# Kernel optimization log

Hardware: AMD Instinct MI355X
Metric: run time of the kernel (lower is better)

Reference implementation:

```python
import jax, jax.numpy as jnp
import numpy as np

N = 100000      # nodes
E = 1600000     # edges (before self loops)
F_IN = 128      # input features
HID = 64        # hidden_layer (heads=1)
G = 128         # number of graphs
NUM_CLASSES = 10


def _gat_layer(x, src, dst, W, a_src, a_dst, b):
    # x: [N, Fin] -> h: [N, HID]; single head, PyG GATConv defaults
    h = x @ W
    alpha_src = h @ a_src            # [N]
    alpha_dst = h @ a_dst            # [N]
    e = jax.nn.leaky_relu(alpha_src[src] + alpha_dst[dst], 0.2)   # [E+N]
    # segment softmax over incoming edges of each destination node
    m = jax.ops.segment_max(e, dst, num_segments=N)
    ex = jnp.exp(e - m[dst])
    denom = jax.ops.segment_sum(ex, dst, num_segments=N)
    alpha = ex / denom[dst]
    out = jax.ops.segment_sum(h[src] * alpha[:, None], dst, num_segments=N)
    return out + b


def setup_inputs() -> dict:
    key = jax.random.key(0)
    ks = jax.random.split(key, 16)
    x = jax.random.normal(ks[0], (N, F_IN), dtype=jnp.float32)
    edge_index = jax.random.randint(ks[1], (2, E), 0, N, dtype=jnp.int64)
    edge_weight = jax.random.uniform(ks[2], (E,), dtype=jnp.float32)
    batch = jnp.sort(jax.random.randint(ks[3], (N,), 0, G, dtype=jnp.int64))
    s = 0.1
    params = {
        'W1': jax.random.normal(ks[4], (F_IN, HID), jnp.float32) * s,
        'a_src1': jax.random.normal(ks[5], (HID,), jnp.float32) * s,
        'a_dst1': jax.random.normal(ks[6], (HID,), jnp.float32) * s,
        'b1': jnp.zeros((HID,), jnp.float32),
        'W2': jax.random.normal(ks[7], (HID, HID), jnp.float32) * s,
        'a_src2': jax.random.normal(ks[8], (HID,), jnp.float32) * s,
        'a_dst2': jax.random.normal(ks[9], (HID,), jnp.float32) * s,
        'b2': jnp.zeros((HID,), jnp.float32),
        'lin_w': jax.random.normal(ks[10], (HID, HID // 2), jnp.float32) * s,
        'lin_b': jnp.zeros((HID // 2,), jnp.float32),
        'cls_w': jax.random.normal(ks[11], (HID // 2, NUM_CLASSES), jnp.float32) * s,
        'cls_b': jnp.zeros((NUM_CLASSES,), jnp.float32),
    }
    return {'x': x, 'edge_index': edge_index, 'edge_weight': edge_weight, 'batch': batch, **params}


def reference(x, edge_index, edge_weight, batch,
              W1, a_src1, a_dst1, b1,
              W2, a_src2, a_dst2, b2,
              lin_w, lin_b, cls_w, cls_b):
    # PyG GATConv add_self_loops=True
    loops = jnp.arange(N, dtype=edge_index.dtype)
    src = jnp.concatenate([edge_index[0], loops])
    dst = jnp.concatenate([edge_index[1], loops])
    # edge_weight unused: GATConv built without edge_dim (lin_edge is None)
    h = _gat_layer(x, src, dst, W1, a_src1, a_dst1, b1)
    h = jax.nn.relu(h)
    h = _gat_layer(h, src, dst, W2, a_src2, a_dst2, b2)
    # global_mean_pool over graphs
    counts = jax.ops.segment_sum(jnp.ones((N,), h.dtype), batch, num_segments=G)
    pooled = jax.ops.segment_sum(h, batch, num_segments=G) / jnp.maximum(counts, 1.0)[:, None]
    z = jax.nn.relu(pooled @ lin_w + lin_b)       # dropout p=0 -> identity
    logits = z @ cls_w + cls_b
    return jax.nn.log_softmax(logits, axis=1)     # SSL=False -> deg_pred=0 omitted
```

## Files before the change

### kernel.cpp

```cpp
#include <hip/hip_runtime.h>
#include <hip/hip_bf16.h>

#define NN 100000
#define NE 1600000
#define NT (NE + NN)
#define FIN 128
#define HID 64
#define NG 128
#define NC 10
#define BSHIFT 8
#define NBUCK ((NN + 255) >> 8)
#define A2_EPB 4096
#define PCH 8

typedef __hip_bfloat16 bf16;

__device__ __forceinline__ float ldx(const void* p, size_t i, int f32flag) {
    return f32flag ? ((const float*)p)[i]
                   : __bfloat162float(((const bf16*)p)[i]);
}
__device__ __forceinline__ float b2f(unsigned short u) {
    return __uint_as_float((unsigned)u << 16);
}
__device__ __forceinline__ unsigned short f2b(float v) {
    return (unsigned short)(__float_as_uint(v) >> 16);
}

__global__ __launch_bounds__(256) void setup_kernel(
        const unsigned int* __restrict__ xw, const int* __restrict__ ei,
        const void* p0, const void* p1, const void* p2, const void* p3,
        const void* p4, const void* p5, const void* p6, const void* p7,
        const void* p8, const void* p9, const void* p10, const void* p11,
        int* __restrict__ flags, int* __restrict__ gcnt, float* __restrict__ Pf) {
    __shared__ int sf[2];
    if (threadIdx.x == 0) {
        int f32 = 0;
        for (int i = 0; i < 64; i++) {
            unsigned int u = xw[i];
            float vl = __uint_as_float((u & 0xffffu) << 16);
            float vh = __uint_as_float(u & 0xffff0000u);
            if (!(fabsf(vl) < 1e10f)) f32 = 1;
            if (!(fabsf(vh) < 1e10f)) f32 = 1;
        }
        int i64 = 1;
        for (int i = 0; i < 64; i++)
            if (ei[2 * i + 1] != 0) i64 = 0;
        sf[0] = f32; sf[1] = i64;
        flags[0] = f32; flags[1] = i64;
    }
    for (int i = threadIdx.x; i < NBUCK; i += 256) gcnt[i] = 0;
    __syncthreads();
    const int f = sf[0];
    const void* ps[12] = {p0,p1,p2,p3,p4,p5,p6,p7,p8,p9,p10,p11};
    const int   sz[12] = {8192,64,64,64,4096,64,64,64,2048,32,320,10};
    int off = 0;
    for (int t = 0; t < 12; t++) {
        for (int i = threadIdx.x; i < sz[t]; i += 256)
            Pf[off + i] = ldx(ps[t], i, f);
        off += sz[t];
    }
}

template <int K>
__global__ __launch_bounds__(256) void gemm_kernel(const void* __restrict__ X,
                                                   const float* __restrict__ Wf,
                                                   const float* __restrict__ va,
                                                   const float* __restrict__ vb,
                                                   unsigned char* __restrict__ H8,
                                                   float* __restrict__ AS,
                                                   float* __restrict__ AD,
                                                   const int* __restrict__ flags,
                                                   int dtype_mode) {
    constexpr int KC = 32;
    constexpr int XLD = KC + 4;
    __shared__ float Wl[KC * HID];
    __shared__ float Xl[64 * XLD];
    const int t = threadIdx.x;
    const int f = (dtype_mode < 0) ? flags[0] : dtype_mode;
    const int brow = blockIdx.x * 64;
    const int rt = (t >> 4) * 4;
    const int ct = (t & 15) * 4;
    float acc[4][4] = {};
    for (int kc = 0; kc < K; kc += KC) {
        for (int i = t; i < KC * HID / 4; i += 256)
            ((float4*)Wl)[i] = ((const float4*)(Wf + kc * HID))[i];
        for (int i = t; i < 64 * KC / 4; i += 256) {
            int rr = i >> 3, col = (i & 7) * 4;
            int grow = brow + rr; if (grow >= NN) grow = NN - 1;
            size_t gbase = (size_t)grow * K + kc + col;
            float4 o;
            if (f) {
                o = *(const float4*)((const float*)X + gbase);
            } else {
                ushort4 v = *(const ushort4*)((const bf16*)X + gbase);
                o.x = b2f(v.x); o.y = b2f(v.y); o.z = b2f(v.z); o.w = b2f(v.w);
            }
            *(float4*)&Xl[rr * XLD + col] = o;
        }
        __syncthreads();
        const float* xp = &Xl[rt * XLD];
        const float* wp = &Wl[ct];
#pragma unroll 2
        for (int k = 0; k < KC; k += 4) {
            float4 w0 = *(const float4*)(wp + (k + 0) * HID);
            float4 w1 = *(const float4*)(wp + (k + 1) * HID);
            float4 w2 = *(const float4*)(wp + (k + 2) * HID);
            float4 w3 = *(const float4*)(wp + (k + 3) * HID);
#pragma unroll
            for (int i = 0; i < 4; i++) {
                float4 xv = *(const float4*)(xp + i * XLD + k);
                acc[i][0] += xv.x * w0.x + xv.y * w1.x + xv.z * w2.x + xv.w * w3.x;
                acc[i][1] += xv.x * w0.y + xv.y * w1.y + xv.z * w2.y + xv.w * w3.y;
                acc[i][2] += xv.x * w0.z + xv.y * w1.z + xv.z * w2.z + xv.w * w3.z;
                acc[i][3] += xv.x * w0.w + xv.y * w1.w + xv.z * w2.w + xv.w * w3.w;
            }
        }
        __syncthreads();
    }
    float va4[4], vb4[4];
#pragma unroll
    for (int j = 0; j < 4; j++) { va4[j] = va[ct + j]; vb4[j] = vb[ct + j]; }
#pragma unroll
    for (int i = 0; i < 4; i++) {
        int row = brow + rt + i;
        unsigned pk = 0;
#pragma unroll
        for (int j = 0; j < 4; j++) {
            int q = (int)rintf(fminf(fmaxf(acc[i][j] * 16.f, -128.f), 127.f)) + 128;
            pk |= ((unsigned)q & 0xffu) << (8 * j);
        }
        if (row < NN)
            *(unsigned*)&H8[((unsigned)row << 6) | ct] = pk;
        float s1 = acc[i][0] * va4[0] + acc[i][1] * va4[1] + acc[i][2] * va4[2] + acc[i][3] * va4[3];
        float s2 = acc[i][0] * vb4[0] + acc[i][1] * vb4[1] + acc[i][2] * vb4[2] + acc[i][3] * vb4[3];
#pragma unroll
        for (int off = 8; off; off >>= 1) {
            s1 += __shfl_xor(s1, off);
            s2 += __shfl_xor(s2, off);
        }
        if ((t & 15) == 0 && row < NN) { AS[row] = s1; AD[row] = s2; }
    }
}

__global__ __launch_bounds__(256) void bhistA_kernel(const int* __restrict__ ei,
                                                     const int* __restrict__ flags,
                                                     int* __restrict__ gcnt) {
    __shared__ int lc[NBUCK];
    for (int i = threadIdx.x; i < NBUCK; i += 256) lc[i] = 0;
    __syncthreads();
    const int i64 = flags[1];
    const int base = blockIdx.x * 8192;
    for (int i = threadIdx.x; i < 8192; i += 256) {
        int e = base + i;
        if (e >= NT) break;
        int d;
        if (e < NE) { long idx = (long)NE + e; d = i64 ? ei[2 * idx] : ei[idx]; }
        else d = e - NE;
        if ((unsigned)d >= NN) d = 0;
        atomicAdd(&lc[d >> BSHIFT], 1);
    }
    __syncthreads();
    for (int i = threadIdx.x; i < NBUCK; i += 256)
        if (lc[i]) atomicAdd(&gcnt[i], lc[i]);
}

__global__ __launch_bounds__(64) void bscan_kernel(const int* __restrict__ gcnt,
                                                   int* __restrict__ gbase,
                                                   int* __restrict__ gcursor) {
    const int lane = threadIdx.x;
    int carry = 0;
    for (int base = 0; base < NBUCK; base += 64) {
        int idx = base + lane;
        int v = (idx < NBUCK) ? gcnt[idx] : 0;
        int x = v;
#pragma unroll
        for (int off = 1; off < 64; off <<= 1) {
            int y = __shfl_up(x, off);
            if (lane >= off) x += y;
        }
        int excl = carry + x - v;
        if (idx < NBUCK) { gbase[idx] = excl; gcursor[idx] = excl; }
        carry += __shfl(x, 63);
    }
    if (lane == 0) gbase[NBUCK] = carry;
}

__global__ __launch_bounds__(256) void bscat_kernel(const int* __restrict__ ei,
                                                    const int* __restrict__ flags,
                                                    int* __restrict__ gcursor,
                                                    int* __restrict__ bucketA) {
    __shared__ int lc[NBUCK];
    __shared__ int lpos[NBUCK];
    __shared__ int lcur[NBUCK];
    for (int i = threadIdx.x; i < NBUCK; i += 256) { lc[i] = 0; lcur[i] = 0; }
    __syncthreads();
    const int i64 = flags[1];
    const int base = blockIdx.x * A2_EPB;
    int sarr[16], darr[16];
#pragma unroll
    for (int i = 0; i < 16; i++) {
        int e = base + i * 256 + threadIdx.x;
        int s = -1, d = 0;
        if (e < NT) {
            if (e < NE) {
                s = i64 ? ei[2 * (long)e] : ei[e];
                long idx = (long)NE + e;
                d = i64 ? ei[2 * idx] : ei[idx];
            } else s = d = e - NE;
            if ((unsigned)d >= NN) d = 0;
            if ((unsigned)s >= NN) s = 0;
            atomicAdd(&lc[d >> BSHIFT], 1);
        }
        sarr[i] = s; darr[i] = d;
    }
    __syncthreads();
    for (int i = threadIdx.x; i < NBUCK; i += 256)
        lpos[i] = lc[i] ? atomicAdd(&gcursor[i], lc[i]) : 0;
    __syncthreads();
#pragma unroll
    for (int i = 0; i < 16; i++) {
        if (sarr[i] >= 0) {
            int b = darr[i] >> BSHIFT;
            int off = atomicAdd(&lcur[b], 1);
            bucketA[lpos[b] + off] = ((darr[i] & 0xff) << 17) | sarr[i];
        }
    }
}

__global__ __launch_bounds__(256) void csr_kernel(const int* __restrict__ bucketA,
                                                  const int* __restrict__ gbase,
                                                  int* __restrict__ rowptr,
                                                  int* __restrict__ slot) {
    const int b = blockIdx.x;
    const int nbase = b << BSHIFT;
    const int nb = min(256, NN - nbase);
    const int ebeg = gbase[b], eend = gbase[b + 1];
    __shared__ int cnt[256];
    __shared__ int excl[257];
    __shared__ int cur[256];
    const int t = threadIdx.x;
    cnt[t] = 0; cur[t] = 0;
    __syncthreads();
    for (int i = ebeg + t; i < eend; i += 256)
        atomicAdd(&cnt[bucketA[i] >> 17], 1);
    __syncthreads();
    if (t < 64) {
        int carry = 0;
        for (int s0 = 0; s0 < 256; s0 += 64) {
            int v = cnt[s0 + t];
            int x = v;
#pragma unroll
            for (int off = 1; off < 64; off <<= 1) {
                int y = __shfl_up(x, off);
                if (t >= off) x += y;
            }
            excl[s0 + t] = carry + x - v;
            carry += __shfl(x, 63);
        }
        if (t == 0) excl[256] = carry;
    }
    __syncthreads();
    if (t < nb) rowptr[nbase + t] = ebeg + excl[t];
    if (b == NBUCK - 1 && t == 0) rowptr[NN] = ebeg + excl[nb];
    for (int i = ebeg + t; i < eend; i += 256) {
        int v = bucketA[i];
        int dl = v >> 17;
        int pos = atomicAdd(&cur[dl], 1);
        slot[ebeg + excl[dl] + pos] = v & 0x1ffff;
    }
}

__global__ __launch_bounds__(256) void edge_kernel(const unsigned char* __restrict__ H8,
                                                   const float* __restrict__ AS,
                                                   const float* __restrict__ AD,
                                                   const int* __restrict__ rowptr,
                                                   const int* __restrict__ slot,
                                                   const float* __restrict__ bias,
                                                   bf16* __restrict__ OUT,
                                                   int relu_flag) {
    int wid = (blockIdx.x * 256 + threadIdx.x) >> 6;
    int lane = threadIdx.x & 63;
    if (wid >= NN) return;
    const int beg = rowptr[wid], end = rowptr[wid + 1];
    const float ad = AD[wid];
    const int sub = lane >> 4;
    const unsigned fq = (unsigned)(lane & 15) * 4u;
    float a0 = 0.f, a1 = 0.f, a2 = 0.f, a3 = 0.f, dsum = 0.f;
    for (int cbeg = beg; cbeg < end; cbeg += 64) {
        int j = cbeg + lane;
        float ex = 0.f; int s = 0;
        if (j < end) {
            s = slot[(unsigned)j];
            float e = AS[(unsigned)s] + ad;
            e = e > 0.f ? e : 0.2f * e;
            ex = __expf(e);
            dsum += ex;
        }
        int cn = min(64, end - cbeg);
        for (int u = 0; u < cn; u += 16) {
            int   s0 = __shfl(s,  u + sub);
            int   s1 = __shfl(s,  u + 4  + sub);
            int   s2 = __shfl(s,  u + 8  + sub);
            int   s3 = __shfl(s,  u + 12 + sub);
            float e0 = __shfl(ex, u + sub);
            float e1 = __shfl(ex, u + 4  + sub);
            float e2 = __shfl(ex, u + 8  + sub);
            float e3 = __shfl(ex, u + 12 + sub);
            unsigned w0 = *(const unsigned*)(H8 + (((unsigned)s0 << 6) | fq));
            unsigned w1 = *(const unsigned*)(H8 + (((unsigned)s1 << 6) | fq));
            unsigned w2 = *(const unsigned*)(H8 + (((unsigned)s2 << 6) | fq));
            unsigned w3 = *(const unsigned*)(H8 + (((unsigned)s3 << 6) | fq));
            a0 += e0 * (float)( w0        & 0xffu);
            a1 += e0 * (float)((w0 >>  8) & 0xffu);
            a2 += e0 * (float)((w0 >> 16) & 0xffu);
            a3 += e0 * (float)( w0 >> 24        );
            a0 += e1 * (float)( w1        & 0xffu);
            a1 += e1 * (float)((w1 >>  8) & 0xffu);
            a2 += e1 * (float)((w1 >> 16) & 0xffu);
            a3 += e1 * (float)( w1 >> 24        );
            a0 += e2 * (float)( w2        & 0xffu);
            a1 += e2 * (float)((w2 >>  8) & 0xffu);
            a2 += e2 * (float)((w2 >> 16) & 0xffu);
            a3 += e2 * (float)( w2 >> 24        );
            a0 += e3 * (float)( w3        & 0xffu);
            a1 += e3 * (float)((w3 >>  8) & 0xffu);
            a2 += e3 * (float)((w3 >> 16) & 0xffu);
            a3 += e3 * (float)( w3 >> 24        );
        }
    }
    a0 += __shfl_xor(a0, 16); a0 += __shfl_xor(a0, 32);
    a1 += __shfl_xor(a1, 16); a1 += __shfl_xor(a1, 32);
    a2 += __shfl_xor(a2, 16); a2 += __shfl_xor(a2, 32);
    a3 += __shfl_xor(a3, 16); a3 += __shfl_xor(a3, 32);
#pragma unroll
    for (int off = 32; off; off >>= 1) dsum += __shfl_xor(dsum, off);
    if (lane < 16) {
        float inv = 0.0625f / dsum;
        float ox = a0 * inv - 8.f + bias[fq + 0];
        float oy = a1 * inv - 8.f + bias[fq + 1];
        float oz = a2 * inv - 8.f + bias[fq + 2];
        float ow = a3 * inv - 8.f + bias[fq + 3];
        if (relu_flag) {
            ox = fmaxf(ox, 0.f); oy = fmaxf(oy, 0.f);
            oz = fmaxf(oz, 0.f); ow = fmaxf(ow, 0.f);
        }
        ushort4 pk;
        pk.x = f2b(ox); pk.y = f2b(oy); pk.z = f2b(oz); pk.w = f2b(ow);
        *(ushort4*)&OUT[((unsigned)wid << 6) | fq] = pk;
    }
}

__global__ __launch_bounds__(256) void pool2a_kernel(const bf16* __restrict__ O,
                                                     const int* __restrict__ bat,
                                                     const int* __restrict__ flags,
                                                     float* __restrict__ part) {
    const int g = blockIdx.x / PCH;
    const int c = blockIdx.x % PCH;
    const int t = threadIdx.x;
    __shared__ int bnds[2];
    if (t < 2) {
        const int i64 = flags[1];
        int target = g + t;
        int lo = 0, hi = NN;
        while (lo < hi) {
            int mid = (lo + hi) >> 1;
            int v = i64 ? bat[2 * (long)mid] : bat[mid];
            if (v < target) lo = mid + 1; else hi = mid;
        }
        bnds[t] = lo;
    }
    __syncthreads();
    const int gbeg = bnds[0], gend = bnds[1];
    const int len = gend - gbeg;
    const int beg = gbeg + (int)((long)len * c / PCH);
    const int end = gbeg + (int)((long)len * (c + 1) / PCH);
    const int lane = t & 63;
    const int wv = t >> 6;
    float acc = 0.f;
    for (int i = beg + wv; i < end; i += 4)
        acc += __bfloat162float(O[((unsigned)i << 6) | (unsigned)lane]);
    __shared__ float red[4][64];
    red[wv][lane] = acc;
    __syncthreads();
    if (wv == 0)
        part[(size_t)(g * PCH + c) * HID + lane] =
            red[0][lane] + red[1][lane] + red[2][lane] + red[3][lane];
}

__global__ __launch_bounds__(64) void tail_kernel(const float* __restrict__ part,
                                                  const int* __restrict__ bat,
                                                  const int* __restrict__ flags,
                                                  const float* __restrict__ lw, const float* __restrict__ lb,
                                                  const float* __restrict__ cw, const float* __restrict__ cb,
                                                  float* __restrict__ out) {
    const int g = blockIdx.x;
    const int t = threadIdx.x;
    __shared__ int bnds[2];
    __shared__ float p[HID];
    __shared__ float z[32];
    __shared__ float lg[NC];
    if (t < 2) {
        const int i64 = flags[1];
        int target = g + t;
        int lo = 0, hi = NN;
        while (lo < hi) {
            int mid = (lo + hi) >> 1;
            int v = i64 ? bat[2 * (long)mid] : bat[mid];
            if (v < target) lo = mid + 1; else hi = mid;
        }
        bnds[t] = lo;
    }
    __syncthreads();
    float s0 = 0.f;
#pragma unroll
    for (int c = 0; c < PCH; c++)
        s0 += part[(size_t)(g * PCH + c) * HID + t];
    float cntg = (float)(bnds[1] - bnds[0]);
    p[t] = s0 / fmaxf(cntg, 1.f);
    __syncthreads();
    if (t < 32) {
        float acc = lb[t];
#pragma unroll
        for (int k = 0; k < HID; k++) acc += p[k] * lw[k * 32 + t];
        z[t] = fmaxf(acc, 0.f);
    }
    __syncthreads();
    if (t < NC) {
        float acc = cb[t];
#pragma unroll
        for (int j = 0; j < 32; j++) acc += z[j] * cw[j * NC + t];
        lg[t] = acc;
    }
    __syncthreads();
    if (t < NC) {
        float mx = -1e30f;
#pragma unroll
        for (int c = 0; c < NC; c++) mx = fmaxf(mx, lg[c]);
        float s = 0.f;
#pragma unroll
        for (int c = 0; c < NC; c++) s += __expf(lg[c] - mx);
        out[g * NC + t] = lg[t] - mx - __logf(s);
    }
}

extern "C" void kernel_launch(void* const* d_in, const int* in_sizes, int n_in,
                              void* d_out, int out_size, void* d_ws, size_t ws_size,
                              hipStream_t stream) {
    const void* x   = d_in[0];
    const int*  ei  = (const int*)d_in[1];
    const int*  bat = (const int*)d_in[3];

    char* w = (char*)d_ws;
    int* bucketA  = (int*)w;   w += sizeof(int) * NT;
    unsigned char* H8 = (unsigned char*)w; w += sizeof(char) * NN * HID;
    bf16* Obf     = (bf16*)w;  w += sizeof(bf16) * NN * HID;
    float* AS     = (float*)w; w += sizeof(float) * NN;
    float* AD     = (float*)w; w += sizeof(float) * NN;
    int* rowptr   = (int*)w;   w += sizeof(int) * (NN + 1);
    int* slot     = (int*)w;   w += sizeof(int) * NT;
    float* part   = (float*)w; w += sizeof(float) * NG * PCH * HID;
    int* gcnt     = (int*)w;   w += sizeof(int) * NBUCK;
    int* gbase    = (int*)w;   w += sizeof(int) * (NBUCK + 1);
    int* gcursor  = (int*)w;   w += sizeof(int) * NBUCK;
    int* flags    = (int*)w;   w += sizeof(int) * 2;
    float* Pf     = (float*)w; w += sizeof(float) * 16384;

    float* W1f = Pf;             float* as1 = Pf + 8192;
    float* ad1 = Pf + 8256;      float* b1  = Pf + 8320;
    float* W2f = Pf + 8384;      float* as2 = Pf + 12480;
    float* ad2 = Pf + 12544;     float* b2  = Pf + 12608;
    float* lw  = Pf + 12672;     float* lb  = Pf + 14720;
    float* cw  = Pf + 14752;     float* cb  = Pf + 15072;

    setup_kernel<<<1, 256, 0, stream>>>((const unsigned int*)x, ei,
                                        d_in[4], d_in[5], d_in[6], d_in[7],
                                        d_in[8], d_in[9], d_in[10], d_in[11],
                                        d_in[12], d_in[13], d_in[14], d_in[15],
                                        flags, gcnt, Pf);
    bhistA_kernel<<<(NT + 8191) / 8192, 256, 0, stream>>>(ei, flags, gcnt);
    bscan_kernel<<<1, 64, 0, stream>>>(gcnt, gbase, gcursor);
    bscat_kernel<<<(NT + A2_EPB - 1) / A2_EPB, 256, 0, stream>>>(ei, flags, gcursor, bucketA);
    csr_kernel<<<NBUCK, 256, 0, stream>>>(bucketA, gbase, rowptr, slot);
    gemm_kernel<FIN><<<(NN + 63) / 64, 256, 0, stream>>>(x, W1f, as1, ad1, H8, AS, AD, flags, -1);
    edge_kernel<<<NN / 4, 256, 0, stream>>>(H8, AS, AD, rowptr, slot, b1, Obf, 1);
    gemm_kernel<HID><<<(NN + 63) / 64, 256, 0, stream>>>(Obf, W2f, as2, ad2, H8, AS, AD, flags, 0);
    edge_kernel<<<NN / 4, 256, 0, stream>>>(H8, AS, AD, rowptr, slot, b2, Obf, 0);
    pool2a_kernel<<<NG * PCH, 256, 0, stream>>>(Obf, bat, flags, part);
    tail_kernel<<<NG, 64, 0, stream>>>(part, bat, flags, lw, lb, cw, cb, (float*)d_out);
}
```

Baseline: 247.9 us.

## Double-buffer GEMM shared-memory tiles with register prefetch of next K chunk

The feature-projection GEMM now keeps two shared-memory buffers for the W and X tiles. The next K chunk is loaded from global memory into registers while the current chunk is being computed, and those registers are written to the other buffer before the barrier. This hides global load latency behind the FMA loop and removes one barrier per iteration. In exchange it doubles shared memory per block and holds more live registers, which may lower occupancy. The GEMM is a small part of a pipeline dominated by edge gathers.

```diff
diff --git a/kernel.cpp b/kernel.cpp
--- a/kernel.cpp
+++ b/kernel.cpp
@@ -73,33 +73,54 @@
                                                    int dtype_mode) {
     constexpr int KC = 32;
     constexpr int XLD = KC + 4;
-    __shared__ float Wl[KC * HID];
-    __shared__ float Xl[64 * XLD];
+    __shared__ float Wl[2][KC * HID];
+    __shared__ float Xl[2][64 * XLD];
     const int t = threadIdx.x;
     const int f = (dtype_mode < 0) ? flags[0] : dtype_mode;
     const int brow = blockIdx.x * 64;
     const int rt = (t >> 4) * 4;
     const int ct = (t & 15) * 4;
     float acc[4][4] = {};
+
+    int rr0 = t >> 3, col0 = (t & 7) * 4;
+    int rr1 = (t + 256) >> 3, col1 = ((t + 256) & 7) * 4;
+    int grow0 = brow + rr0; if (grow0 >= NN) grow0 = NN - 1;
+    int grow1 = brow + rr1; if (grow1 >= NN) grow1 = NN - 1;
+
+    auto loadX = [&](int kc2, int grow, int col) -> float4 {
+        size_t gbase = (size_t)grow * K + kc2 + col;
+        float4 o;
+        if (f) {
+            o = *(const float4*)((const float*)X + gbase);
+        } else {
+            ushort4 v = *(const ushort4*)((const bf16*)X + gbase);
+            o.x = b2f(v.x); o.y = b2f(v.y); o.z = b2f(v.z); o.w = b2f(v.w);
+        }
+        return o;
+    };
+
+    {
+        ((float4*)Wl[0])[t]       = ((const float4*)Wf)[t];
+        ((float4*)Wl[0])[t + 256] = ((const float4*)Wf)[t + 256];
+        *(float4*)&Xl[0][rr0 * XLD + col0] = loadX(0, grow0, col0);
+        *(float4*)&Xl[0][rr1 * XLD + col1] = loadX(0, grow1, col1);
+    }
+    __syncthreads();
+
+    int cur = 0;
     for (int kc = 0; kc < K; kc += KC) {
-        for (int i = t; i < KC * HID / 4; i += 256)
-            ((float4*)Wl)[i] = ((const float4*)(Wf + kc * HID))[i];
-        for (int i = t; i < 64 * KC / 4; i += 256) {
-            int rr = i >> 3, col = (i & 7) * 4;
-            int grow = brow + rr; if (grow >= NN) grow = NN - 1;
-            size_t gbase = (size_t)grow * K + kc + col;
-            float4 o;
-            if (f) {
-                o = *(const float4*)((const float*)X + gbase);
-            } else {
-                ushort4 v = *(const ushort4*)((const bf16*)X + gbase);
-                o.x = b2f(v.x); o.y = b2f(v.y); o.z = b2f(v.z); o.w = b2f(v.w);
-            }
-            *(float4*)&Xl[rr * XLD + col] = o;
-        }
-        __syncthreads();
-        const float* xp = &Xl[rt * XLD];
-        const float* wp = &Wl[ct];
+        const int nxt = cur ^ 1;
+        const bool pre = (kc + KC) < K;
+        float4 wr0, wr1, xr0, xr1;
+        if (pre) {
+            const float4* wsrc = (const float4*)(Wf + (kc + KC) * HID);
+            wr0 = wsrc[t];
+            wr1 = wsrc[t + 256];
+            xr0 = loadX(kc + KC, grow0, col0);
+            xr1 = loadX(kc + KC, grow1, col1);
+        }
+        const float* xp = &Xl[cur][rt * XLD];
+        const float* wp = &Wl[cur][ct];
 #pragma unroll 2
         for (int k = 0; k < KC; k += 4) {
             float4 w0 = *(const float4*)(wp + (k + 0) * HID);
@@ -115,8 +136,16 @@
                 acc[i][3] += xv.x * w0.w + xv.y * w1.w + xv.z * w2.w + xv.w * w3.w;
             }
         }
+        if (pre) {
+            ((float4*)Wl[nxt])[t]       = wr0;
+            ((float4*)Wl[nxt])[t + 256] = wr1;
+            *(float4*)&Xl[nxt][rr0 * XLD + col0] = xr0;
+            *(float4*)&Xl[nxt][rr1 * XLD + col1] = xr1;
+        }
         __syncthreads();
-    }
+        cur = nxt;
+    }
+
     float va4[4], vb4[4];
 #pragma unroll
     for (int j = 0; j < 4; j++) { va4[j] = va[ct + j]; vb4[j] = vb[ct + j]; }
```

Result: slower. 254.9 us (+2.8%).
